# Optimization experiments

Measured on AMD Instinct MI355X. Metric: run time of the kernel, lower is better.

## Reference

```python
import jax, jax.numpy as jnp
import numpy as np

DIM = 512
HEADS = 8
DIM_HEAD = 32
INNER = HEADS * DIM_HEAD  # 256
B, N = 2, 2048
EPS = 1e-5


def setup_inputs() -> dict:
    key = jax.random.key(0)
    ks = jax.random.split(key, 6)
    x = jax.random.normal(ks[0], (B, N, DIM), dtype=jnp.float32)
    rel_pos_bias = jax.random.normal(ks[1], (HEADS, N, N), dtype=jnp.float32)
    ln_scale = jnp.ones((DIM,), dtype=jnp.float32)
    w_qkv = jax.random.normal(ks[2], (DIM, INNER * 3), dtype=jnp.float32) / np.sqrt(DIM)
    w_out = jax.random.normal(ks[3], (INNER, DIM), dtype=jnp.float32) / np.sqrt(INNER)
    b_out = jnp.zeros((DIM,), dtype=jnp.float32)
    return {"x": x, "rel_pos_bias": rel_pos_bias, "ln_scale": ln_scale,
            "w_qkv": w_qkv, "w_out": w_out, "b_out": b_out}


def reference(x, rel_pos_bias, ln_scale, w_qkv, w_out, b_out):
    scale = DIM_HEAD ** -0.5
    # LayerNorm (no bias), eps=1e-5
    mu = jnp.mean(x, axis=-1, keepdims=True)
    var = jnp.mean(jnp.square(x - mu), axis=-1, keepdims=True)
    xn = (x - mu) * jax.lax.rsqrt(var + EPS) * ln_scale
    # fused QKV projection, no bias
    qkv = xn @ w_qkv  # [b, n, 3*inner]
    q, k, v = jnp.split(qkv, 3, axis=-1)
    def to_heads(t):
        b, n, _ = t.shape
        return t.reshape(b, n, HEADS, DIM_HEAD).transpose(0, 2, 1, 3)  # b h n d
    q, k, v = map(to_heads, (q, k, v))
    q = q * scale
    sim = jnp.einsum('bhid,bhjd->bhij', q, k)
    sim = sim + rel_pos_bias  # (h,n,n) broadcasts over batch
    attn = jax.nn.softmax(sim, axis=-1)
    o = jnp.einsum('bhij,bhjd->bhid', attn, v)
    o = o.transpose(0, 2, 1, 3).reshape(x.shape[0], x.shape[1], INNER)  # b n (h d)
    return o @ w_out + b_out
```

## Files before the change

### kernel.cpp

```cpp
#include <hip/hip_runtime.h>
#include <hip/hip_bf16.h>
#include <cstdint>

#define NB 2
#define NSEQ 2048
#define NSEQP 2176
#define NDIM 512
#define NHEAD 8
#define DHEAD 32
#define NINNER 256
#define NQKV 768
#define LNEPS 1e-5f
#define QSCALE 0.17677669529663687f

typedef short short8 __attribute__((ext_vector_type(8)));
typedef float f32x4 __attribute__((ext_vector_type(4)));
typedef unsigned int u32x4 __attribute__((ext_vector_type(4)));
typedef unsigned int u32x2 __attribute__((ext_vector_type(2)));
typedef unsigned short u16;
typedef unsigned int u32;

__device__ __forceinline__ f32x4 mfma16(short8 a, short8 b, f32x4 c) {
    return __builtin_amdgcn_mfma_f32_16x16x32_bf16(a, b, c, 0, 0, 0);
}

__device__ __forceinline__ u16 f2bf(float a) {
    union { float f; u32 u; } x; x.f = a;
    u32 r = x.u + 0x7fffu + ((x.u >> 16) & 1u);
    return (u16)(r >> 16);
}
__device__ __forceinline__ float bf2f(u16 h) {
    union { float f; u32 u; } x; x.u = ((u32)h) << 16; return x.f;
}
__device__ __forceinline__ void split2(float a, u16& hi, u16& lo) {
    hi = f2bf(a);
    lo = f2bf(a - bf2f(hi));
}
__device__ __forceinline__ u32 pk2(float a, float b) {
    return (u32)f2bf(a) | ((u32)f2bf(b) << 16);
}

__global__ __launch_bounds__(256) void ln_kernel(
    const float* __restrict__ x, const float* __restrict__ gamma,
    u32* __restrict__ xn_hi, u32* __restrict__ xn_lo)
{
    const int row = blockIdx.x;
    const int t = threadIdx.x;
    const float2 v = ((const float2*)(x + (size_t)row * NDIM))[t];
    float s1 = v.x + v.y;
    float s2 = v.x * v.x + v.y * v.y;
    #pragma unroll
    for (int off = 32; off >= 1; off >>= 1) {
        s1 += __shfl_down(s1, off);
        s2 += __shfl_down(s2, off);
    }
    __shared__ float a1[4], a2[4];
    if ((t & 63) == 0) { a1[t >> 6] = s1; a2[t >> 6] = s2; }
    __syncthreads();
    const float ts1 = a1[0] + a1[1] + a1[2] + a1[3];
    const float ts2 = a2[0] + a2[1] + a2[2] + a2[3];
    const float mu = ts1 * (1.0f / NDIM);
    const float var = ts2 * (1.0f / NDIM) - mu * mu;
    const float rs = rsqrtf(var + LNEPS);
    const float2 g = ((const float2*)gamma)[t];
    u16 h0, l0, h1, l1;
    split2((v.x - mu) * rs * g.x, h0, l0);
    split2((v.y - mu) * rs * g.y, h1, l1);
    xn_hi[(size_t)row * (NDIM / 2) + t] = (u32)h0 | ((u32)h1 << 16);
    xn_lo[(size_t)row * (NDIM / 2) + t] = (u32)l0 | ((u32)l1 << 16);
}

__global__ __launch_bounds__(256) void wtrans_kernel(
    const float* __restrict__ wq, u16* __restrict__ wqT_hi, u16* __restrict__ wqT_lo,
    const float* __restrict__ wo, u16* __restrict__ woT_hi, u16* __restrict__ woT_lo)
{
    __shared__ __align__(16) u16 th[64][72], tl[64][72];
    const int t = threadIdx.x;
    const float* w; u16 *wT_hi, *wT_lo; int K, N, k0, n0;
    if (blockIdx.x < 96) {
        w = wq; wT_hi = wqT_hi; wT_lo = wqT_lo; K = NDIM; N = NQKV;
        k0 = (blockIdx.x & 7) * 64; n0 = (blockIdx.x >> 3) * 64;
    } else {
        const int b = blockIdx.x - 96;
        w = wo; wT_hi = woT_hi; wT_lo = woT_lo; K = NINNER; N = NDIM;
        k0 = (b & 3) * 64; n0 = (b >> 2) * 64;
    }
    {
        const int k = t >> 2, c = (t & 3) * 16;
        const float* src = w + (size_t)(k0 + k) * N + n0 + c;
        #pragma unroll
        for (int jj = 0; jj < 4; jj++) {
            const f32x4 w4 = *(const f32x4*)(src + jj * 4);
            #pragma unroll
            for (int e = 0; e < 4; e++) {
                u16 hh, ll;
                split2(w4[e], hh, ll);
                th[k][c + jj * 4 + e] = hh;
                tl[k][c + jj * 4 + e] = ll;
            }
        }
    }
    __syncthreads();
    {
        const int n = t >> 2, kc = (t & 3) * 16;
        u16 hb[16], lb[16];
        #pragma unroll
        for (int j = 0; j < 16; j++) { hb[j] = th[kc + j][n]; lb[j] = tl[kc + j][n]; }
        u16* dh = wT_hi + (size_t)(n0 + n) * K + k0 + kc;
        u16* dl = wT_lo + (size_t)(n0 + n) * K + k0 + kc;
        *(short8*)dh = *(short8*)hb;
        *(short8*)(dh + 8) = *(short8*)(hb + 8);
        *(short8*)dl = *(short8*)lb;
        *(short8*)(dl + 8) = *(short8*)(lb + 8);
    }
}

__global__ __launch_bounds__(256) void vtrans_kernel(
    const u16* __restrict__ v, u16* __restrict__ vt)
{
    __shared__ __align__(16) u16 sh[64][40];
    const int t = threadIdx.x;
    const int n0 = blockIdx.x * 64;
    const int bh = blockIdx.y;
    {
        const int n = t >> 2, c = (t & 3) * 8;
        *(short8*)&sh[n][c] = *(const short8*)(v + ((size_t)bh * NSEQ + n0 + n) * DHEAD + c);
    }
    __syncthreads();
    {
        const int d = t >> 3, nc = (t & 7) * 8;
        u16 buf[8];
        #pragma unroll
        for (int j = 0; j < 8; j++) buf[j] = sh[nc + j][d];
        *(short8*)(vt + ((size_t)bh * DHEAD + d) * NSEQP + n0 + nc) = *(short8*)buf;
    }
}

__global__ __launch_bounds__(256, 4) void qkv_kernel(
    const u16* __restrict__ xn_hi, const u16* __restrict__ xn_lo,
    const u16* __restrict__ wT_hi, const u16* __restrict__ wT_lo,
    u16* __restrict__ q_hi, u16* __restrict__ q_lo,
    u16* __restrict__ k_hi, u16* __restrict__ k_lo,
    u16* __restrict__ v)
{
    __shared__ __align__(16) u16 Ah[64][40], Al[64][40], Bh[64][40], Bl[64][40];
    const int t = threadIdx.x;
    const int wave = t >> 6, lane = t & 63;
    const int lrow = lane & 15, lquad = lane >> 4;
    const int rowBase = blockIdx.x * 64;
    const int colBase = blockIdx.y * 64;
    const int wm = (wave & 1) * 32;
    const int wn = (wave >> 1) * 32;
    const int kf = lquad * 8;
    const f32x4 zero = {0.f, 0.f, 0.f, 0.f};
    f32x4 acc[2][2];
    acc[0][0] = zero; acc[0][1] = zero; acc[1][0] = zero; acc[1][1] = zero;

    const int sr = t >> 2, sc = (t & 3) * 8;

    for (int k0 = 0; k0 < NDIM; k0 += 32) {
        __syncthreads();
        *(short8*)&Ah[sr][sc] = *(const short8*)(xn_hi + (size_t)(rowBase + sr) * NDIM + k0 + sc);
        *(short8*)&Al[sr][sc] = *(const short8*)(xn_lo + (size_t)(rowBase + sr) * NDIM + k0 + sc);
        *(short8*)&Bh[sr][sc] = *(const short8*)(wT_hi + (size_t)(colBase + sr) * NDIM + k0 + sc);
        *(short8*)&Bl[sr][sc] = *(const short8*)(wT_lo + (size_t)(colBase + sr) * NDIM + k0 + sc);
        __syncthreads();
        const short8 a0h = *(const short8*)&Ah[wm + lrow][kf];
        const short8 a0l = *(const short8*)&Al[wm + lrow][kf];
        const short8 a1h = *(const short8*)&Ah[wm + 16 + lrow][kf];
        const short8 a1l = *(const short8*)&Al[wm + 16 + lrow][kf];
        const short8 b0h = *(const short8*)&Bh[wn + lrow][kf];
        const short8 b0l = *(const short8*)&Bl[wn + lrow][kf];
        const short8 b1h = *(const short8*)&Bh[wn + 16 + lrow][kf];
        const short8 b1l = *(const short8*)&Bl[wn + 16 + lrow][kf];
        acc[0][0] = mfma16(a0h, b0h, acc[0][0]); acc[0][0] = mfma16(a0h, b0l, acc[0][0]); acc[0][0] = mfma16(a0l, b0h, acc[0][0]);
        acc[0][1] = mfma16(a0h, b1h, acc[0][1]); acc[0][1] = mfma16(a0h, b1l, acc[0][1]); acc[0][1] = mfma16(a0l, b1h, acc[0][1]);
        acc[1][0] = mfma16(a1h, b0h, acc[1][0]); acc[1][0] = mfma16(a1h, b0l, acc[1][0]); acc[1][0] = mfma16(a1l, b0h, acc[1][0]);
        acc[1][1] = mfma16(a1h, b1h, acc[1][1]); acc[1][1] = mfma16(a1h, b1l, acc[1][1]); acc[1][1] = mfma16(a1l, b1h, acc[1][1]);
    }

    #pragma unroll
    for (int mi = 0; mi < 2; mi++) {
        #pragma unroll
        for (int ni = 0; ni < 2; ni++) {
            #pragma unroll
            for (int r = 0; r < 4; r++) {
                const int grow = rowBase + wm + mi * 16 + lquad * 4 + r;
                const int gcol = colBase + wn + ni * 16 + lrow;
                const float val = acc[mi][ni][r];
                const int bidx = grow >> 11;
                const int n = grow & (NSEQ - 1);
                const int sec = gcol >> 8;
                const int idx = gcol & 255;
                const int head = idx >> 5, d = idx & 31;
                const int bh = bidx * NHEAD + head;
                if (sec == 0) {
                    u16 hh, ll;
                    split2(val * QSCALE, hh, ll);
                    const size_t a = ((size_t)bh * NSEQ + n) * DHEAD + d;
                    q_hi[a] = hh; q_lo[a] = ll;
                } else if (sec == 1) {
                    u16 hh, ll;
                    split2(val, hh, ll);
                    const size_t a = ((size_t)bh * NSEQ + n) * DHEAD + d;
                    k_hi[a] = hh; k_lo[a] = ll;
                } else {
                    v[((size_t)bh * NSEQ + n) * DHEAD + d] = f2bf(val);
                }
            }
        }
    }
}

__global__ __launch_bounds__(512) void attn_kernel(
    const u16* __restrict__ q_hi, const u16* __restrict__ q_lo,
    const u16* __restrict__ k_hi, const u16* __restrict__ k_lo,
    const u16* __restrict__ vt,
    const float* __restrict__ bias,
    u16* __restrict__ o_hi, u16* __restrict__ o_lo)
{
    __shared__ __align__(16) float bs_lds[32][132];
    __shared__ __align__(16) float cA[2][4][64][4];
    __shared__ __align__(16) float cB[2][4][64][4];
    __shared__ float cl[2][4][16];
    const int t = threadIdx.x;
    const int wave = t >> 6, lane = t & 63;
    const int lrow = lane & 15, lquad = lane >> 4;
    const int qpair = wave & 1, ksub = wave >> 1;
    const int bh = blockIdx.y;
    const int batch = bh >> 3, head = bh & 7;
    const int qb = blockIdx.x * 32;
    const size_t qkb = (size_t)bh * NSEQ * DHEAD;
    const size_t vtb = (size_t)bh * DHEAD * NSEQP;
    const size_t qoff = (size_t)(qb + qpair * 16 + lrow) * DHEAD + lquad * 8;
    const short8 qh = *(const short8*)(q_hi + qkb + qoff);
    const short8 ql = *(const short8*)(q_lo + qkb + qoff);
    const f32x4 zero = {0.f, 0.f, 0.f, 0.f};
    f32x4 accA = zero, accB = zero;
    float lp = 0.f;
    const int kperm = ((lrow >> 2) << 3) | (lrow & 3);
    const int srow = t >> 4, scol = (t & 15) * 8;
    const float* bsrc = bias + (size_t)head * NSEQ * NSEQ + (size_t)(qb + srow) * NSEQ + scol;

    {
        const f32x4 r0 = *(const f32x4*)(bsrc);
        const f32x4 r1 = *(const f32x4*)(bsrc + 4);
        *(f32x4*)&bs_lds[srow][scol] = r0;
        *(f32x4*)&bs_lds[srow][scol + 4] = r1;
    }
    __syncthreads();

    for (int i = 0; i < 16; i++) {
        const int kt = i * 128 + ksub * 32;
        const size_t kof = (size_t)(kt + kperm) * DHEAD + lquad * 8;
        const short8 k0h = *(const short8*)(k_hi + qkb + kof);
        const short8 k0l = *(const short8*)(k_lo + qkb + kof);
        const short8 k1h = *(const short8*)(k_hi + qkb + kof + 4 * DHEAD);
        const short8 k1l = *(const short8*)(k_lo + qkb + kof + 4 * DHEAD);
        const short8 va0 = *(const short8*)(vt + vtb + (size_t)lrow * NSEQP + kt + lquad * 8);
        const short8 va1 = *(const short8*)(vt + vtb + (size_t)(16 + lrow) * NSEQP + kt + lquad * 8);
        f32x4 n0 = zero, n1 = zero;
        if (i < 15) {
            n0 = *(const f32x4*)(bsrc + (i + 1) * 128);
            n1 = *(const f32x4*)(bsrc + (i + 1) * 128 + 4);
        }
        const int brow = qpair * 16 + lrow;
        const int bcol = ksub * 32 + lquad * 8;
        const f32x4 b00 = *(const f32x4*)&bs_lds[brow][bcol];
        const f32x4 b01 = *(const f32x4*)&bs_lds[brow][bcol + 4];

        f32x4 c0 = zero, c1 = zero;
        c0 = mfma16(k0h, qh, c0); c0 = mfma16(k0h, ql, c0); c0 = mfma16(k0l, qh, c0);
        c1 = mfma16(k1h, qh, c1); c1 = mfma16(k1h, ql, c1); c1 = mfma16(k1l, qh, c1);
        f32x4 p0, p1;
        #pragma unroll
        for (int r = 0; r < 4; r++) {
            p0[r] = __expf(c0[r] + b00[r]);
            p1[r] = __expf(c1[r] + b01[r]);
        }
        lp += (p0[0] + p0[1]) + (p0[2] + p0[3]) + (p1[0] + p1[1]) + (p1[2] + p1[3]);
        union { u32x4 u; short8 s; } cv;
        cv.u[0] = pk2(p0[0], p0[1]);
        cv.u[1] = pk2(p0[2], p0[3]);
        cv.u[2] = pk2(p1[0], p1[1]);
        cv.u[3] = pk2(p1[2], p1[3]);
        accA = mfma16(va0, cv.s, accA);
        accB = mfma16(va1, cv.s, accB);

        __syncthreads();
        if (i < 15) {
            *(f32x4*)&bs_lds[srow][scol] = n0;
            *(f32x4*)&bs_lds[srow][scol + 4] = n1;
        }
        __syncthreads();
    }

    lp += __shfl_xor(lp, 16); lp += __shfl_xor(lp, 32);

    *(f32x4*)&cA[qpair][ksub][lane][0] = accA;
    *(f32x4*)&cB[qpair][ksub][lane][0] = accB;
    if (lquad == 0) {
        cl[qpair][ksub][lrow] = lp;
    }
    __syncthreads();
    if (wave < 4) {
        const int s = wave >> 1, part = wave & 1;
        const float (*src)[64][4] = part ? (const float (*)[64][4])cB[s]
                                         : (const float (*)[64][4])cA[s];
        f32x4 sv = *(const f32x4*)&src[0][lane][0];
        #pragma unroll
        for (int w = 1; w < 4; w++) {
            sv += *(const f32x4*)&src[w][lane][0];
        }
        float lt = 0.f;
        #pragma unroll
        for (int w = 0; w < 4; w++) lt += cl[s][w][lrow];
        const float inv = 1.0f / lt;
        const int q = qb + s * 16 + lrow;
        const size_t base = ((size_t)batch * NSEQ + q) * NINNER + head * DHEAD + part * 16 + lquad * 4;
        u16 h[4], l[4];
        #pragma unroll
        for (int r = 0; r < 4; r++) {
            split2(sv[r] * inv, h[r], l[r]);
        }
        *(u32x2*)&o_hi[base] = *(u32x2*)&h[0];
        *(u32x2*)&o_lo[base] = *(u32x2*)&l[0];
    }
}

__global__ __launch_bounds__(256, 4) void out_kernel(
    const u16* __restrict__ o_hi, const u16* __restrict__ o_lo,
    const u16* __restrict__ wT_hi, const u16* __restrict__ wT_lo,
    const float* __restrict__ b_out,
    float* __restrict__ out)
{
    __shared__ __align__(16) u16 Ah[64][40], Al[64][40], Bh[64][40], Bl[64][40];
    const int t = threadIdx.x;
    const int wave = t >> 6, lane = t & 63;
    const int lrow = lane & 15, lquad = lane >> 4;
    const int rowBase = blockIdx.x * 64;
    const int colBase = blockIdx.y * 64;
    const int wm = (wave & 1) * 32;
    const int wn = (wave >> 1) * 32;
    const int kf = lquad * 8;
    const f32x4 zero = {0.f, 0.f, 0.f, 0.f};
    f32x4 acc[2][2];
    acc[0][0] = zero; acc[0][1] = zero; acc[1][0] = zero; acc[1][1] = zero;

    const int sr = t >> 2, sc = (t & 3) * 8;

    for (int k0 = 0; k0 < NINNER; k0 += 32) {
        __syncthreads();
        *(short8*)&Ah[sr][sc] = *(const short8*)(o_hi + (size_t)(rowBase + sr) * NINNER + k0 + sc);
        *(short8*)&Al[sr][sc] = *(const short8*)(o_lo + (size_t)(rowBase + sr) * NINNER + k0 + sc);
        *(short8*)&Bh[sr][sc] = *(const short8*)(wT_hi + (size_t)(colBase + sr) * NINNER + k0 + sc);
        *(short8*)&Bl[sr][sc] = *(const short8*)(wT_lo + (size_t)(colBase + sr) * NINNER + k0 + sc);
        __syncthreads();
        const short8 a0h = *(const short8*)&Ah[wm + lrow][kf];
        const short8 a0l = *(const short8*)&Al[wm + lrow][kf];
        const short8 a1h = *(const short8*)&Ah[wm + 16 + lrow][kf];
        const short8 a1l = *(const short8*)&Al[wm + 16 + lrow][kf];
        const short8 b0h = *(const short8*)&Bh[wn + lrow][kf];
        const short8 b0l = *(const short8*)&Bl[wn + lrow][kf];
        const short8 b1h = *(const short8*)&Bh[wn + 16 + lrow][kf];
        const short8 b1l = *(const short8*)&Bl[wn + 16 + lrow][kf];
        acc[0][0] = mfma16(a0h, b0h, acc[0][0]); acc[0][0] = mfma16(a0h, b0l, acc[0][0]); acc[0][0] = mfma16(a0l, b0h, acc[0][0]);
        acc[0][1] = mfma16(a0h, b1h, acc[0][1]); acc[0][1] = mfma16(a0h, b1l, acc[0][1]); acc[0][1] = mfma16(a0l, b1h, acc[0][1]);
        acc[1][0] = mfma16(a1h, b0h, acc[1][0]); acc[1][0] = mfma16(a1h, b0l, acc[1][0]); acc[1][0] = mfma16(a1l, b0h, acc[1][0]);
        acc[1][1] = mfma16(a1h, b1h, acc[1][1]); acc[1][1] = mfma16(a1h, b1l, acc[1][1]); acc[1][1] = mfma16(a1l, b1h, acc[1][1]);
    }

    #pragma unroll
    for (int mi = 0; mi < 2; mi++) {
        #pragma unroll
        for (int ni = 0; ni < 2; ni++) {
            #pragma unroll
            for (int r = 0; r < 4; r++) {
                const int grow = rowBase + wm + mi * 16 + lquad * 4 + r;
                const int gcol = colBase + wn + ni * 16 + lrow;
                out[(size_t)grow * NDIM + gcol] = acc[mi][ni][r] + b_out[gcol];
            }
        }
    }
}

extern "C" void kernel_launch(void* const* d_in, const int* in_sizes, int n_in,
                              void* d_out, int out_size, void* d_ws, size_t ws_size,
                              hipStream_t stream)
{
    (void)in_sizes; (void)n_in; (void)out_size; (void)ws_size;
    const float* x     = (const float*)d_in[0];
    const float* bias  = (const float*)d_in[1];
    const float* gamma = (const float*)d_in[2];
    const float* wqkv  = (const float*)d_in[3];
    const float* wout  = (const float*)d_in[4];
    const float* bout  = (const float*)d_in[5];
    float* out = (float*)d_out;

    char* ws = (char*)d_ws;
    size_t off = 0;
    auto carve = [&](size_t bytes) -> void* {
        void* p = (void*)(ws + off);
        off += (bytes + 255) & ~(size_t)255;
        return p;
    };
    const size_t rows = (size_t)NB * NSEQ;
    const size_t hn = (size_t)NB * NHEAD * NSEQ * DHEAD;
    const size_t hnp = (size_t)NB * NHEAD * DHEAD * NSEQP;
    u16* xn_hi = (u16*)carve(rows * NDIM * 2);
    u16* xn_lo = (u16*)carve(rows * NDIM * 2);
    u16* wqT_hi = (u16*)carve((size_t)NQKV * NDIM * 2);
    u16* wqT_lo = (u16*)carve((size_t)NQKV * NDIM * 2);
    u16* woT_hi = (u16*)carve((size_t)NDIM * NINNER * 2);
    u16* woT_lo = (u16*)carve((size_t)NDIM * NINNER * 2);
    u16* q_hi  = (u16*)carve(hn * 2);
    u16* q_lo  = (u16*)carve(hn * 2);
    u16* k_hi  = (u16*)carve(hn * 2);
    u16* k_lo  = (u16*)carve(hn * 2);
    u16* vbuf  = (u16*)carve(hn * 2);
    u16* vt    = (u16*)carve(hnp * 2);
    u16* o_hi  = (u16*)carve(rows * NINNER * 2);
    u16* o_lo  = (u16*)carve(rows * NINNER * 2);

    ln_kernel<<<dim3((unsigned)rows), 256, 0, stream>>>(x, gamma, (u32*)xn_hi, (u32*)xn_lo);
    wtrans_kernel<<<dim3(128), 256, 0, stream>>>(wqkv, wqT_hi, wqT_lo, wout, woT_hi, woT_lo);
    qkv_kernel<<<dim3(64, 12), 256, 0, stream>>>(xn_hi, xn_lo, wqT_hi, wqT_lo,
                                                 q_hi, q_lo, k_hi, k_lo, vbuf);
    vtrans_kernel<<<dim3(NSEQ / 64, NB * NHEAD), 256, 0, stream>>>(vbuf, vt);
    attn_kernel<<<dim3(NSEQ / 32, NB * NHEAD), 512, 0, stream>>>(q_hi, q_lo, k_hi, k_lo,
                                                                 vt, bias, o_hi, o_lo);
    out_kernel<<<dim3(64, 8), 256, 0, stream>>>(o_hi, o_lo, woT_hi, woT_lo, bout, out);
}
```

Before: 286.3 us.

## Split keys across waves with 64-query tiles and direct bias loads

The attention kernel now gives each of the 8 waves a contiguous 256-key slice and has every wave process four 16-query fragments. Each K/V fragment load is therefore reused across 64 queries instead of 16. The bias tile is read straight from global memory into registers, which removes the LDS staging and the two block barriers per iteration. The cost is higher register pressure, a larger 8-way cross-wave reduction through LDS, half as many blocks, and removal of the padded V-transpose stride, which may bring back cache or channel conflicts.

Result: no change. 287.1 us (+0.3%).

```diff
diff --git a/kernel.cpp b/kernel.cpp
--- a/kernel.cpp
+++ b/kernel.cpp
@@ -4,7 +4,6 @@
 
 #define NB 2
 #define NSEQ 2048
-#define NSEQP 2176
 #define NDIM 512
 #define NHEAD 8
 #define DHEAD 32
@@ -132,7 +131,7 @@
         u16 buf[8];
         #pragma unroll
         for (int j = 0; j < 8; j++) buf[j] = sh[nc + j][d];
-        *(short8*)(vt + ((size_t)bh * DHEAD + d) * NSEQP + n0 + nc) = *(short8*)buf;
+        *(short8*)(vt + ((size_t)bh * DHEAD + d) * NSEQ + n0 + nc) = *(short8*)buf;
     }
 }
 
@@ -219,104 +218,109 @@
     const float* __restrict__ bias,
     u16* __restrict__ o_hi, u16* __restrict__ o_lo)
 {
-    __shared__ __align__(16) float bs_lds[32][132];
-    __shared__ __align__(16) float cA[2][4][64][4];
-    __shared__ __align__(16) float cB[2][4][64][4];
-    __shared__ float cl[2][4][16];
+    __shared__ __align__(16) float cbuf[4][8][64][4];
+    __shared__ float cl[4][8][16];
     const int t = threadIdx.x;
     const int wave = t >> 6, lane = t & 63;
     const int lrow = lane & 15, lquad = lane >> 4;
-    const int qpair = wave & 1, ksub = wave >> 1;
+    const int kslice = wave;
     const int bh = blockIdx.y;
     const int batch = bh >> 3, head = bh & 7;
-    const int qb = blockIdx.x * 32;
+    const int qb = blockIdx.x * 64;
     const size_t qkb = (size_t)bh * NSEQ * DHEAD;
-    const size_t vtb = (size_t)bh * DHEAD * NSEQP;
-    const size_t qoff = (size_t)(qb + qpair * 16 + lrow) * DHEAD + lquad * 8;
-    const short8 qh = *(const short8*)(q_hi + qkb + qoff);
-    const short8 ql = *(const short8*)(q_lo + qkb + qoff);
+    short8 qh[4], ql[4];
+    #pragma unroll
+    for (int f = 0; f < 4; f++) {
+        const size_t qoff = (size_t)(qb + f * 16 + lrow) * DHEAD + lquad * 8;
+        qh[f] = *(const short8*)(q_hi + qkb + qoff);
+        ql[f] = *(const short8*)(q_lo + qkb + qoff);
+    }
     const f32x4 zero = {0.f, 0.f, 0.f, 0.f};
-    f32x4 accA = zero, accB = zero;
-    float lp = 0.f;
+    f32x4 accA[4], accB[4];
+    float lp[4];
+    #pragma unroll
+    for (int f = 0; f < 4; f++) { accA[f] = zero; accB[f] = zero; lp[f] = 0.f; }
     const int kperm = ((lrow >> 2) << 3) | (lrow & 3);
-    const int srow = t >> 4, scol = (t & 15) * 8;
-    const float* bsrc = bias + (size_t)head * NSEQ * NSEQ + (size_t)(qb + srow) * NSEQ + scol;
-
-    {
-        const f32x4 r0 = *(const f32x4*)(bsrc);
-        const f32x4 r1 = *(const f32x4*)(bsrc + 4);
-        *(f32x4*)&bs_lds[srow][scol] = r0;
-        *(f32x4*)&bs_lds[srow][scol + 4] = r1;
-    }
-    __syncthreads();
-
-    for (int i = 0; i < 16; i++) {
-        const int kt = i * 128 + ksub * 32;
+    const float* bbase = bias + (size_t)head * NSEQ * NSEQ + (size_t)(qb + lrow) * NSEQ;
+    const int kt0 = kslice * 256;
+
+    for (int i = 0; i < 8; i++) {
+        const int kt = kt0 + i * 32;
         const size_t kof = (size_t)(kt + kperm) * DHEAD + lquad * 8;
         const short8 k0h = *(const short8*)(k_hi + qkb + kof);
         const short8 k0l = *(const short8*)(k_lo + qkb + kof);
         const short8 k1h = *(const short8*)(k_hi + qkb + kof + 4 * DHEAD);
         const short8 k1l = *(const short8*)(k_lo + qkb + kof + 4 * DHEAD);
-        const short8 va0 = *(const short8*)(vt + vtb + (size_t)lrow * NSEQP + kt + lquad * 8);
-        const short8 va1 = *(const short8*)(vt + vtb + (size_t)(16 + lrow) * NSEQP + kt + lquad * 8);
-        f32x4 n0 = zero, n1 = zero;
-        if (i < 15) {
-            n0 = *(const f32x4*)(bsrc + (i + 1) * 128);
-            n1 = *(const f32x4*)(bsrc + (i + 1) * 128 + 4);
+        const short8 va0 = *(const short8*)(vt + qkb + (size_t)lrow * NSEQ + kt + lquad * 8);
+        const short8 va1 = *(const short8*)(vt + qkb + (size_t)(16 + lrow) * NSEQ + kt + lquad * 8);
+
+        #pragma unroll
+        for (int f = 0; f < 4; f++) {
+            const float* bp = bbase + (size_t)f * 16 * NSEQ + kt + lquad * 8;
+            const f32x4 b0 = *(const f32x4*)bp;
+            const f32x4 b1 = *(const f32x4*)(bp + 4);
+            f32x4 c0 = zero, c1 = zero;
+            c0 = mfma16(k0h, qh[f], c0); c0 = mfma16(k0h, ql[f], c0); c0 = mfma16(k0l, qh[f], c0);
+            c1 = mfma16(k1h, qh[f], c1); c1 = mfma16(k1h, ql[f], c1); c1 = mfma16(k1l, qh[f], c1);
+            f32x4 p0, p1;
+            #pragma unroll
+            for (int r = 0; r < 4; r++) {
+                p0[r] = __expf(c0[r] + b0[r]);
+                p1[r] = __expf(c1[r] + b1[r]);
+            }
+            lp[f] += (p0[0] + p0[1]) + (p0[2] + p0[3]) + (p1[0] + p1[1]) + (p1[2] + p1[3]);
+            union { u32x4 u; short8 s; } cv;
+            cv.u[0] = pk2(p0[0], p0[1]);
+            cv.u[1] = pk2(p0[2], p0[3]);
+            cv.u[2] = pk2(p1[0], p1[1]);
+            cv.u[3] = pk2(p1[2], p1[3]);
+            accA[f] = mfma16(va0, cv.s, accA[f]);
+            accB[f] = mfma16(va1, cv.s, accB[f]);
         }
-        const int brow = qpair * 16 + lrow;
-        const int bcol = ksub * 32 + lquad * 8;
-        const f32x4 b00 = *(const f32x4*)&bs_lds[brow][bcol];
-        const f32x4 b01 = *(const f32x4*)&bs_lds[brow][bcol + 4];
-
-        f32x4 c0 = zero, c1 = zero;
-        c0 = mfma16(k0h, qh, c0); c0 = mfma16(k0h, ql, c0); c0 = mfma16(k0l, qh, c0);
-        c1 = mfma16(k1h, qh, c1); c1 = mfma16(k1h, ql, c1); c1 = mfma16(k1l, qh, c1);
-        f32x4 p0, p1;
-        #pragma unroll
-        for (int r = 0; r < 4; r++) {
-            p0[r] = __expf(c0[r] + b00[r]);
-            p1[r] = __expf(c1[r] + b01[r]);
-        }
-        lp += (p0[0] + p0[1]) + (p0[2] + p0[3]) + (p1[0] + p1[1]) + (p1[2] + p1[3]);
-        union { u32x4 u; short8 s; } cv;
-        cv.u[0] = pk2(p0[0], p0[1]);
-        cv.u[1] = pk2(p0[2], p0[3]);
-        cv.u[2] = pk2(p1[0], p1[1]);
-        cv.u[3] = pk2(p1[2], p1[3]);
-        accA = mfma16(va0, cv.s, accA);
-        accB = mfma16(va1, cv.s, accB);
-
-        __syncthreads();
-        if (i < 15) {
-            *(f32x4*)&bs_lds[srow][scol] = n0;
-            *(f32x4*)&bs_lds[srow][scol + 4] = n1;
-        }
-        __syncthreads();
-    }
-
-    lp += __shfl_xor(lp, 16); lp += __shfl_xor(lp, 32);
-
-    *(f32x4*)&cA[qpair][ksub][lane][0] = accA;
-    *(f32x4*)&cB[qpair][ksub][lane][0] = accB;
+    }
+
+    #pragma unroll
+    for (int f = 0; f < 4; f++) {
+        lp[f] += __shfl_xor(lp[f], 16);
+        lp[f] += __shfl_xor(lp[f], 32);
+    }
+
+    #pragma unroll
+    for (int f = 0; f < 4; f++)
+        *(f32x4*)&cbuf[f][kslice][lane][0] = accA[f];
     if (lquad == 0) {
-        cl[qpair][ksub][lrow] = lp;
-    }
-    __syncthreads();
+        #pragma unroll
+        for (int f = 0; f < 4; f++) cl[f][kslice][lrow] = lp[f];
+    }
+    __syncthreads();
+    f32x4 sv = zero;
+    float lt = 0.f;
     if (wave < 4) {
-        const int s = wave >> 1, part = wave & 1;
-        const float (*src)[64][4] = part ? (const float (*)[64][4])cB[s]
-                                         : (const float (*)[64][4])cA[s];
-        f32x4 sv = *(const f32x4*)&src[0][lane][0];
-        #pragma unroll
-        for (int w = 1; w < 4; w++) {
-            sv += *(const f32x4*)&src[w][lane][0];
-        }
-        float lt = 0.f;
-        #pragma unroll
-        for (int w = 0; w < 4; w++) lt += cl[s][w][lrow];
+        const int f = wave;
+        sv = *(const f32x4*)&cbuf[f][0][lane][0];
+        #pragma unroll
+        for (int w = 1; w < 8; w++) sv += *(const f32x4*)&cbuf[f][w][lane][0];
+        #pragma unroll
+        for (int w = 0; w < 8; w++) lt += cl[f][w][lrow];
+    }
+    __syncthreads();
+    #pragma unroll
+    for (int f = 0; f < 4; f++)
+        *(f32x4*)&cbuf[f][kslice][lane][0] = accB[f];
+    __syncthreads();
+    if (wave >= 4) {
+        const int f = wave - 4;
+        sv = *(const f32x4*)&cbuf[f][0][lane][0];
+        #pragma unroll
+        for (int w = 1; w < 8; w++) sv += *(const f32x4*)&cbuf[f][w][lane][0];
+        #pragma unroll
+        for (int w = 0; w < 8; w++) lt += cl[f][w][lrow];
+    }
+    {
+        const int f = (wave < 4) ? wave : (wave - 4);
+        const int part = (wave < 4) ? 0 : 1;
         const float inv = 1.0f / lt;
-        const int q = qb + s * 16 + lrow;
+        const int q = qb + f * 16 + lrow;
         const size_t base = ((size_t)batch * NSEQ + q) * NINNER + head * DHEAD + part * 16 + lquad * 4;
         u16 h[4], l[4];
         #pragma unroll
@@ -406,7 +410,6 @@
     };
     const size_t rows = (size_t)NB * NSEQ;
     const size_t hn = (size_t)NB * NHEAD * NSEQ * DHEAD;
-    const size_t hnp = (size_t)NB * NHEAD * DHEAD * NSEQP;
     u16* xn_hi = (u16*)carve(rows * NDIM * 2);
     u16* xn_lo = (u16*)carve(rows * NDIM * 2);
     u16* wqT_hi = (u16*)carve((size_t)NQKV * NDIM * 2);
@@ -418,7 +421,7 @@
     u16* k_hi  = (u16*)carve(hn * 2);
     u16* k_lo  = (u16*)carve(hn * 2);
     u16* vbuf  = (u16*)carve(hn * 2);
-    u16* vt    = (u16*)carve(hnp * 2);
+    u16* vt    = (u16*)carve(hn * 2);
     u16* o_hi  = (u16*)carve(rows * NINNER * 2);
     u16* o_lo  = (u16*)carve(rows * NINNER * 2);
 
@@ -427,7 +430,7 @@
     qkv_kernel<<<dim3(64, 12), 256, 0, stream>>>(xn_hi, xn_lo, wqT_hi, wqT_lo,
                                                  q_hi, q_lo, k_hi, k_lo, vbuf);
     vtrans_kernel<<<dim3(NSEQ / 64, NB * NHEAD), 256, 0, stream>>>(vbuf, vt);
-    attn_kernel<<<dim3(NSEQ / 32, NB * NHEAD), 512, 0, stream>>>(q_hi, q_lo, k_hi, k_lo,
+    attn_kernel<<<dim3(NSEQ / 64, NB * NHEAD), 512, 0, stream>>>(q_hi, q_lo, k_hi, k_lo,
                                                                  vt, bias, o_hi, o_lo);
     out_kernel<<<dim3(64, 8), 256, 0, stream>>>(o_hi, o_lo, woT_hi, woT_lo, bout, out);
 }
```
